# Performance work log

Hardware: AMD Instinct MI355X
Metric: run time of the kernel (lower is better)

Reference implementation:

```python
import jax, jax.numpy as jnp
import numpy as np

# db4 analysis filters (pywt.Wavelet('db4').dec_lo / dec_hi)
_DEC_LO = np.array([-0.010597401784997278, 0.032883011666982945, 0.030841381835986965,
                    -0.18703481171888114, -0.02798376941698385, 0.6308807679295904,
                    0.7148465705525415, 0.23037781330885523], dtype=np.float32)
_DEC_HI = np.array([-0.23037781330885523, 0.7148465705525415, -0.6308807679295904,
                    -0.02798376941698385, 0.18703481171888114, 0.030841381835986965,
                    -0.032883011666982945, -0.010597401784997278], dtype=np.float32)
# pytorch_wavelets stores filters reversed (torch conv = correlation); lax.conv is
# also correlation, so use the same reversed filters. Shape [2, 1, L].
_H = jnp.asarray(np.stack([_DEC_LO[::-1], _DEC_HI[::-1]])[:, None, :])

B, SW, SWS, HW, K, J = 2048, 4, 64, 8, 128, 3
DWT_LEN = 84  # 14 (lo, level 3) + 35 (hi1) + 21 (hi2) + 14 (hi3)


def _dwt_level(x, h):
    """One analysis level, mode='reflect' (pytorch_wavelets afb1d). x: [M, N]."""
    N = x.shape[-1]
    L = h.shape[-1]
    outsize = (N + L - 1) // 2          # pywt.dwt_coeff_len, non-periodization
    p = 2 * (outsize - 1) - N + L
    if p % 2 == 1:                       # odd total pad: one extra zero at the end
        x = jnp.pad(x, ((0, 0), (0, 1)))
    x = jnp.pad(x, ((0, 0), (p // 2, p // 2)), mode='reflect')
    y = jax.lax.conv_general_dilated(x[:, None, :], h, (2,), 'VALID')  # [M, 2, out]
    return y[:, 0, :], y[:, 1, :]


def setup_inputs() -> dict:
    key = jax.random.key(0)
    k1, k2, k3 = jax.random.split(key, 3)
    x = jax.random.normal(k1, (B, 1, SW * SWS, HW, HW), dtype=jnp.float32)
    # one Conv3d(1 -> K, kernel=(DWT_LEN, 8, 8)) per subwindow, kaiming-ish init
    fan_in = DWT_LEN * HW * HW
    conv_weight = jax.random.normal(k2, (SW, K, DWT_LEN, HW, HW), dtype=jnp.float32) / np.sqrt(fan_in)
    conv_bias = jax.random.normal(k3, (SW, K), dtype=jnp.float32) * 0.01
    return {"x": x, "conv_weight": conv_weight, "conv_bias": conv_bias}


def reference(x, conv_weight, conv_bias):
    b = x.shape[0]
    # [B,1,T,8,8] -> [B,SW,8,8,SWS]: DWT runs along the time axis of each subwindow
    xt = x[:, 0].reshape(b, SW, SWS, HW, HW).transpose(0, 1, 3, 4, 2)
    xm = xt.reshape(-1, SWS)  # [B*SW*64, 64]
    lo, highs = xm, []
    for _ in range(J):
        lo, hi = _dwt_level(lo, _H)
        highs.append(hi)
    coeffs = jnp.concatenate([lo] + highs, axis=-1)  # [M, 84], order: lo, hi1, hi2, hi3
    c = coeffs.reshape(b, SW, HW, HW, DWT_LEN).transpose(0, 1, 4, 2, 3)  # [B,SW,84,8,8]
    # per-subwindow Conv3d that fully reduces (t,h,w) -> [B, SW, K]
    feat = jnp.einsum('bsthw,skthw->bsk', c, conv_weight) + conv_bias[None]
    # Dropout3d is identity in eval; LeakyReLU default slope 0.01 (typo in source
    # means leakyrelu_negative_slope is never applied)
    return jax.nn.leaky_relu(feat, 0.01).reshape(b, SW * K)
```

## Files before the change

kernel.cpp:

```cpp
#include <hip/hip_runtime.h>
#include <stdint.h>

typedef unsigned int   u32;
typedef unsigned short u16;
typedef __bf16 bf16x8 __attribute__((ext_vector_type(8)));
typedef float  f32x4  __attribute__((ext_vector_type(4)));
typedef float  f32x2  __attribute__((ext_vector_type(2)));

struct WdT { float v[84][64]; };

constexpr WdT build_wd() {
    WdT W{};
    const float GLc[8] = { 0.23037781330885523f,  0.7148465705525415f,
                           0.6308807679295904f,  -0.02798376941698385f,
                          -0.18703481171888114f,  0.030841381835986965f,
                           0.032883011666982945f,-0.010597401784997278f };
    const float GHc[8] = {-0.010597401784997278f,-0.032883011666982945f,
                           0.030841381835986965f, 0.18703481171888114f,
                          -0.02798376941698385f, -0.6308807679295904f,
                           0.7148465705525415f,  -0.23037781330885523f };
    for (int j = 0; j < 64; ++j) {
        float lo1[35] = {}, lo2[21] = {};
        for (int i = 0; i < 35; ++i) {
            float sl = 0.f, sh = 0.f;
            for (int t = 0; t < 8; ++t) {
                int s = 2*i + t - 6;
                if (s < 0)   s = -s;
                if (s >= 64) s = 126 - s;
                if (s == j) { sl += GLc[t]; sh += GHc[t]; }
            }
            lo1[i] = sl; W.v[14 + i][j] = sh;
        }
        for (int i = 0; i < 21; ++i) {
            float sl = 0.f, sh = 0.f;
            for (int t = 0; t < 8; ++t) {
                int s = 2*i + t - 6;
                if (s < 0)   s = -s;
                if (s >= 36) s = 70 - s;
                if (s < 35) { sl += lo1[s]*GLc[t]; sh += lo1[s]*GHc[t]; }
            }
            lo2[i] = sl; W.v[49 + i][j] = sh;
        }
        for (int i = 0; i < 14; ++i) {
            float sl = 0.f, sh = 0.f;
            for (int t = 0; t < 8; ++t) {
                int s = 2*i + t - 6;
                if (s < 0)   s = -s;
                if (s >= 22) s = 42 - s;
                if (s < 21) { sl += lo2[s]*GLc[t]; sh += lo2[s]*GHc[t]; }
            }
            W.v[i][j] = sl; W.v[70 + i][j] = sh;
        }
    }
    return W;
}

__constant__ WdT WD = build_wd();

__device__ inline u16 f32_bf16(float f) {
    u32 u = __float_as_uint(f);
    u += 0x7fffu + ((u >> 16) & 1u);
    return (u16)(u >> 16);
}
__device__ inline u32 pack2_bf16(float a, float b) {
    u32 ua = __float_as_uint(a); ua += 0x7fffu + ((ua >> 16) & 1u);
    u32 ub = __float_as_uint(b); ub += 0x7fffu + ((ub >> 16) & 1u);
    return (ua >> 16) | (ub & 0xffff0000u);
}

__global__ __launch_bounds__(256) void fold_w(const float* __restrict__ cw,
                                              u16* __restrict__ Wf) {
    const int tid = threadIdx.x;
    const int sk  = blockIdx.x;
    const int s   = sk >> 7;
    const int n   = sk & 127;
    const int hw  = tid & 63;
    const int tg  = __builtin_amdgcn_readfirstlane((int)(tid >> 6));
    const int t0  = tg * 16;
    const float* wk = cw + (size_t)sk * (84 * 64);

    float acc[16];
#pragma unroll
    for (int j = 0; j < 16; ++j) acc[j] = 0.f;

#pragma unroll 4
    for (int tau = 0; tau < 84; ++tau) {
        const float wv = wk[tau * 64 + hw];
#pragma unroll
        for (int j = 0; j < 16; ++j) acc[j] += wv * WD.v[tau][t0 + j];
    }

    const int nt  = n >> 4;
    const int fr  = n & 15;
    const int fq  = (hw >> 3) & 3;
    const int jj  = hw & 7;
    const int kbh = hw >> 5;
#pragma unroll
    for (int j = 0; j < 16; ++j) {
        const int t = t0 + j;
        const size_t idx =
            ((((size_t)(s * 128 + t * 2 + kbh)) * 8 + nt) * 64 + fq * 16 + fr) * 8 + jj;
        Wf[idx] = f32_bf16(acc[j]);
    }
}

__global__ __launch_bounds__(512, 8) void gemm_f(const float* __restrict__ X,
                                                 const u16* __restrict__ Wf,
                                                 const float* __restrict__ bias,
                                                 float* __restrict__ out) {
    __shared__ __align__(16) float R[16 * 68];
    const int tid  = threadIdx.x;
    const int lane = tid & 63;
    const int w    = tid >> 6;
    const int bid  = blockIdx.x;
    const int wgid = ((bid & 7) << 7) + (bid >> 3);
    const int nh   = wgid & 1;
    const int mt   = (wgid >> 1) & 127;
    const int s    = wgid >> 8;
    const int fr   = lane & 15;
    const int fq   = lane >> 4;
    const int kb0  = w * 16;

    for (int i = tid; i < 16 * 68; i += 512) R[i] = 0.f;
    __syncthreads();

    const float* xg = X + (size_t)(mt * 16 + fr) * 16384 + s * 4096 + kb0 * 32 + fq * 8;
    const f32x4* xa = reinterpret_cast<const f32x4*>(xg);
    const u16*   wg = Wf + ((size_t)(s * 128 + kb0) * 8 + nh * 4) * 512 + lane * 8;

    f32x4 acc[4];
#pragma unroll
    for (int nt = 0; nt < 4; ++nt) acc[nt] = (f32x4){0.f, 0.f, 0.f, 0.f};

#pragma unroll
    for (int kb = 0; kb < 16; ++kb) {
        const f32x4 a0 = xa[kb * 8];
        const f32x4 a1 = xa[kb * 8 + 1];
        union { u32 u[4]; bf16x8 v; } av;
        av.u[0] = pack2_bf16(a0.x, a0.y); av.u[1] = pack2_bf16(a0.z, a0.w);
        av.u[2] = pack2_bf16(a1.x, a1.y); av.u[3] = pack2_bf16(a1.z, a1.w);
        const u16* wb = wg + (size_t)kb * 4096;
#pragma unroll
        for (int nt = 0; nt < 4; ++nt) {
            const bf16x8 bf = *reinterpret_cast<const bf16x8*>(wb + nt * 512);
            acc[nt] = __builtin_amdgcn_mfma_f32_16x16x32_bf16(av.v, bf, acc[nt], 0, 0, 0);
        }
    }

#pragma unroll
    for (int nt = 0; nt < 4; ++nt)
#pragma unroll
        for (int r = 0; r < 4; ++r)
            atomicAdd(&R[(fq * 4 + r) * 68 + nt * 16 + fr], acc[nt][r]);
    __syncthreads();

    {
        const int o     = tid * 2;
        const int row   = o >> 6;
        const int col64 = o & 63;
        const f32x2 v = *reinterpret_cast<const f32x2*>(&R[row * 68 + col64]);
        const f32x2 b = *reinterpret_cast<const f32x2*>(bias + s * 128 + nh * 64 + col64);
        f32x2 u = v + b;
        u.x = u.x > 0.f ? u.x : 0.01f * u.x;
        u.y = u.y > 0.f ? u.y : 0.01f * u.y;
        *reinterpret_cast<f32x2*>(
            out + (size_t)(mt * 16 + row) * 512 + s * 128 + nh * 64 + col64) = u;
    }
}

extern "C" void kernel_launch(void* const* d_in, const int* in_sizes, int n_in,
                              void* d_out, int out_size, void* d_ws, size_t ws_size,
                              hipStream_t stream) {
    const float* x  = (const float*)d_in[0];
    const float* cw = (const float*)d_in[1];
    const float* cb = (const float*)d_in[2];
    float* out = (float*)d_out;

    u16* Wf = (u16*)d_ws;

    fold_w<<<512, 256, 0, stream>>>(cw, Wf);
    gemm_f<<<1024, 512, 0, stream>>>(x, Wf, cb, out);
}
```

Baseline: 258.0 us.

## Restructure GEMM into LDS-staged 128x128 tiles with split-K and reduction kernel

Replaces the 16-row-per-block GEMM, which re-reads the folded weights for every 16-row M tile, with 128x128 output tiles. A and B are staged through double-buffered LDS using global_load_lds with an XOR swizzle, and K is split across blocks (8 or 4 ways depending on workspace). Partial sums go to a workspace buffer and a separate reduce kernel adds bias and applies LeakyReLU. This raises weight reuse and overlaps loads with MFMA, at the cost of extra partial-sum traffic (up to 32 MB written and read back) and one more launch.

```diff
diff --git a/kernel.cpp b/kernel.cpp
--- a/kernel.cpp
+++ b/kernel.cpp
@@ -5,7 +5,6 @@
 typedef unsigned short u16;
 typedef __bf16 bf16x8 __attribute__((ext_vector_type(8)));
 typedef float  f32x4  __attribute__((ext_vector_type(4)));
-typedef float  f32x2  __attribute__((ext_vector_type(2)));
 
 struct WdT { float v[84][64]; };
 
@@ -68,6 +67,12 @@
     return (ua >> 16) | (ub & 0xffff0000u);
 }
 
+typedef const __attribute__((address_space(1))) u32 gas_u32;
+typedef __attribute__((address_space(3)))       u32 las_u32;
+__device__ inline void gl16(const void* g, void* l) {
+    __builtin_amdgcn_global_load_lds((gas_u32*)g, (las_u32*)l, 16, 0, 0);
+}
+
 __global__ __launch_bounds__(256) void fold_w(const float* __restrict__ cw,
                                               u16* __restrict__ Wf) {
     const int tid = threadIdx.x;
@@ -104,68 +109,121 @@
     }
 }
 
-__global__ __launch_bounds__(512, 8) void gemm_f(const float* __restrict__ X,
-                                                 const u16* __restrict__ Wf,
-                                                 const float* __restrict__ bias,
-                                                 float* __restrict__ out) {
-    __shared__ __align__(16) float R[16 * 68];
+template <int KQ>
+__global__ __launch_bounds__(256) void gemm_f(const float* __restrict__ X,
+                                              const u16* __restrict__ Wf,
+                                              float* __restrict__ P) {
+    constexpr int NSTEP = 128 / KQ;
+    __shared__ float As[2][4096];
+    __shared__ u16   Bs[2][4096];
+
     const int tid  = threadIdx.x;
     const int lane = tid & 63;
     const int w    = tid >> 6;
-    const int bid  = blockIdx.x;
-    const int wgid = ((bid & 7) << 7) + (bid >> 3);
-    const int nh   = wgid & 1;
-    const int mt   = (wgid >> 1) & 127;
-    const int s    = wgid >> 8;
+    const int wm   = w >> 1, wn = w & 1;
     const int fr   = lane & 15;
     const int fq   = lane >> 4;
-    const int kb0  = w * 16;
-
-    for (int i = tid; i < 16 * 68; i += 512) R[i] = 0.f;
-    __syncthreads();
-
-    const float* xg = X + (size_t)(mt * 16 + fr) * 16384 + s * 4096 + kb0 * 32 + fq * 8;
-    const f32x4* xa = reinterpret_cast<const f32x4*>(xg);
-    const u16*   wg = Wf + ((size_t)(s * 128 + kb0) * 8 + nh * 4) * 512 + lane * 8;
-
-    f32x4 acc[4];
-#pragma unroll
-    for (int nt = 0; nt < 4; ++nt) acc[nt] = (f32x4){0.f, 0.f, 0.f, 0.f};
-
-#pragma unroll
-    for (int kb = 0; kb < 16; ++kb) {
-        const f32x4 a0 = xa[kb * 8];
-        const f32x4 a1 = xa[kb * 8 + 1];
-        union { u32 u[4]; bf16x8 v; } av;
-        av.u[0] = pack2_bf16(a0.x, a0.y); av.u[1] = pack2_bf16(a0.z, a0.w);
-        av.u[2] = pack2_bf16(a1.x, a1.y); av.u[3] = pack2_bf16(a1.z, a1.w);
-        const u16* wb = wg + (size_t)kb * 4096;
-#pragma unroll
-        for (int nt = 0; nt < 4; ++nt) {
-            const bf16x8 bf = *reinterpret_cast<const bf16x8*>(wb + nt * 512);
-            acc[nt] = __builtin_amdgcn_mfma_f32_16x16x32_bf16(av.v, bf, acc[nt], 0, 0, 0);
-        }
-    }
-
-#pragma unroll
-    for (int nt = 0; nt < 4; ++nt)
-#pragma unroll
-        for (int r = 0; r < 4; ++r)
-            atomicAdd(&R[(fq * 4 + r) * 68 + nt * 16 + fr], acc[nt][r]);
-    __syncthreads();
-
-    {
-        const int o     = tid * 2;
-        const int row   = o >> 6;
-        const int col64 = o & 63;
-        const f32x2 v = *reinterpret_cast<const f32x2*>(&R[row * 68 + col64]);
-        const f32x2 b = *reinterpret_cast<const f32x2*>(bias + s * 128 + nh * 64 + col64);
-        f32x2 u = v + b;
-        u.x = u.x > 0.f ? u.x : 0.01f * u.x;
-        u.y = u.y > 0.f ? u.y : 0.01f * u.y;
-        *reinterpret_cast<f32x2*>(
-            out + (size_t)(mt * 16 + row) * 512 + s * 128 + nh * 64 + col64) = u;
-    }
+
+    const int bid  = blockIdx.x;
+    const int wg   = (bid & 7) * (8 * KQ) + (bid >> 3);
+    const int mt   = wg & 15;
+    const int s    = (wg >> 4) & 3;
+    const int kq   = wg >> 6;
+
+    const int am   = tid >> 3;
+    const int ab   = ((tid & 7) * 16) ^ ((am & 7) << 4);
+    const float* xa = X + (size_t)(mt * 128 + am) * 16384 + s * 4096
+                        + (size_t)kq * (4096 / KQ) + (ab >> 2);
+    const char* wb0 = (const char*)Wf + ((size_t)(s * 128 + kq * NSTEP) << 13)
+                        + (size_t)tid * 16;
+
+    f32x4 acc[4][4];
+#pragma unroll
+    for (int mi = 0; mi < 4; ++mi)
+#pragma unroll
+        for (int ni = 0; ni < 4; ++ni) acc[mi][ni] = (f32x4){0.f, 0.f, 0.f, 0.f};
+
+#define STAGE(buf, step)                                                       \
+    do {                                                                       \
+        char* la = (char*)&As[buf][0] + tid * 16;                              \
+        char* lb = (char*)&Bs[buf][0] + tid * 16;                              \
+        const float* ga = xa + (size_t)(step) * 32;                            \
+        const char*  gb = wb0 + ((size_t)(step) << 13);                        \
+        gl16(ga,            la);                                               \
+        gl16(ga + 524288,   la + 4096);                                        \
+        gl16(ga + 1048576,  la + 8192);                                        \
+        gl16(ga + 1572864,  la + 12288);                                       \
+        gl16(gb,            lb);                                               \
+        gl16(gb + 4096,     lb + 4096);                                        \
+    } while (0)
+
+    STAGE(0, 0);
+    int cur = 0;
+#pragma unroll 1
+    for (int step = 0; step < NSTEP; ++step) {
+        if (step + 1 < NSTEP) {
+            STAGE(cur ^ 1, step + 1);
+            asm volatile("s_waitcnt vmcnt(6)" ::: "memory");
+        } else {
+            asm volatile("s_waitcnt vmcnt(0)" ::: "memory");
+        }
+        __builtin_amdgcn_s_barrier();
+
+        const float* Ab = &As[cur][0];
+        const u16*   Bb = &Bs[cur][0];
+        bf16x8 bfr[4];
+#pragma unroll
+        for (int ni = 0; ni < 4; ++ni)
+            bfr[ni] = *reinterpret_cast<const bf16x8*>(
+                Bb + ((wn * 4 + ni) * 64 + lane) * 8);
+        const int swz = (fr & 7) << 4;
+        const int b0  = (fq * 32) ^ swz;
+        const int b1  = (fq * 32 + 16) ^ swz;
+#pragma unroll
+        for (int mi = 0; mi < 4; ++mi) {
+            const int m = wm * 64 + mi * 16 + fr;
+            const f32x4 r0 = *reinterpret_cast<const f32x4*>(Ab + m * 32 + (b0 >> 2));
+            const f32x4 r1 = *reinterpret_cast<const f32x4*>(Ab + m * 32 + (b1 >> 2));
+            union { u32 u[4]; bf16x8 v; } av;
+            av.u[0] = pack2_bf16(r0.x, r0.y); av.u[1] = pack2_bf16(r0.z, r0.w);
+            av.u[2] = pack2_bf16(r1.x, r1.y); av.u[3] = pack2_bf16(r1.z, r1.w);
+#pragma unroll
+            for (int ni = 0; ni < 4; ++ni)
+                acc[mi][ni] = __builtin_amdgcn_mfma_f32_16x16x32_bf16(
+                    av.v, bfr[ni], acc[mi][ni], 0, 0, 0);
+        }
+        asm volatile("s_waitcnt lgkmcnt(0)" ::: "memory");
+        __builtin_amdgcn_s_barrier();
+        cur ^= 1;
+    }
+#undef STAGE
+
+    float* pg = P + (size_t)kq * (2048 * 512)
+                  + (size_t)(mt * 128 + wm * 64) * 512 + s * 128 + wn * 64 + fr;
+#pragma unroll
+    for (int mi = 0; mi < 4; ++mi)
+#pragma unroll
+        for (int ni = 0; ni < 4; ++ni)
+#pragma unroll
+            for (int r = 0; r < 4; ++r)
+                pg[(size_t)(mi * 16 + fq * 4 + r) * 512 + ni * 16] = acc[mi][ni][r];
+}
+
+__global__ __launch_bounds__(256) void reduce_k(const float* __restrict__ P,
+                                                const float* __restrict__ bias,
+                                                float* __restrict__ out, int nks) {
+    const int t = blockIdx.x * 256 + threadIdx.x;
+    const size_t base = (size_t)t * 4;
+    f32x4 sum = {0.f, 0.f, 0.f, 0.f};
+    for (int k = 0; k < nks; ++k)
+        sum += *reinterpret_cast<const f32x4*>(P + (size_t)k * (2048 * 512) + base);
+    const f32x4 b = *reinterpret_cast<const f32x4*>(bias + (base & 511));
+    f32x4 o = sum + b;
+    o.x = o.x > 0.f ? o.x : 0.01f * o.x;
+    o.y = o.y > 0.f ? o.y : 0.01f * o.y;
+    o.z = o.z > 0.f ? o.z : 0.01f * o.z;
+    o.w = o.w > 0.f ? o.w : 0.01f * o.w;
+    __builtin_nontemporal_store(o, reinterpret_cast<f32x4*>(out + base));
 }
 
 extern "C" void kernel_launch(void* const* d_in, const int* in_sizes, int n_in,
@@ -176,8 +234,16 @@
     const float* cb = (const float*)d_in[2];
     float* out = (float*)d_out;
 
-    u16* Wf = (u16*)d_ws;
-
+    u16*   Wf = (u16*)d_ws;
+    float* P  = (float*)((char*)d_ws + (4u << 20));
+
+    const size_t MN = (size_t)2048 * 512 * 4;
     fold_w<<<512, 256, 0, stream>>>(cw, Wf);
-    gemm_f<<<1024, 512, 0, stream>>>(x, Wf, cb, out);
-}
+    if (ws_size >= (4u << 20) + 8 * MN) {
+        gemm_f<8><<<512, 256, 0, stream>>>(x, Wf, P);
+        reduce_k<<<1024, 256, 0, stream>>>(P, cb, out, 8);
+    } else {
+        gemm_f<4><<<256, 256, 0, stream>>>(x, Wf, P);
+        reduce_k<<<1024, 256, 0, stream>>>(P, cb, out, 4);
+    }
+}
```

New measurement: 233.8 us. 9.4% less time.
